# Optimization experiments

Hardware: AMD Instinct MI355X
Metric: run time of the kernel (lower is better)

The kernel has to match this reference:

```python
import jax, jax.numpy as jnp
import numpy as np
from jax import lax

# --- Clifford algebra Cl(3,0): sig_g = [1,1,1], n_blades = 8 ---
SIG = np.array([1.0, 1.0, 1.0], dtype=np.float32)
N_GEN = len(SIG)
N_BLADES = 1 << N_GEN

def _build_cayley(g):
    # Structure constants C[a,b,c]: e_a * e_b = C[a,b,a^b] * e_{a^b}
    n = len(g); nb = 1 << n
    C = np.zeros((nb, nb, nb), dtype=np.float32)
    for a in range(nb):
        for b in range(nb):
            s = 1.0
            x = a >> 1
            while x:
                if bin(x & b).count('1') % 2:
                    s = -s
                x >>= 1
            common = a & b
            for k in range(n):
                if (common >> k) & 1:
                    s *= g[k]
            C[a, b, a ^ b] = s
    return C

CAYLEY = _build_cayley(SIG)
# blade signs: scalar coefficient of e_i * e_i (metric square of each blade)
BLADE_SIGNS = np.array([CAYLEY[i, i, 0] for i in range(N_BLADES)], dtype=np.float32)

DT = 0.1      # EPEngine dt
N_FREE = 5    # EPEngine n_free

def _energy(h, input_mv, W_rec, C, signs):
    # h: [B,L,H,I]
    rho = jnp.clip(h, 0.0, 1.0)
    E_self = 0.5 * jnp.sum(h * h, axis=(1, 2, 3))                       # [B]
    E_in = jnp.einsum('blhi,blhi,i->b', rho, input_mv, signs)           # [B]
    # causal recurrent term: geometric product of h_{l-1} with W_rec
    rec = jnp.einsum('blhi,ghj,ijk->blgk', rho[:, :-1], W_rec, C)       # [B,L-1,H,I]
    E_rec = jnp.einsum('blhk,blhk,k->b', rho[:, 1:], rec, signs)        # [B]
    return E_self - E_in - E_rec

def _free_phase(h0, input_mv, W_rec, C, signs):
    gfn = jax.grad(lambda h: jnp.sum(_energy(h, input_mv, W_rec, C, signs)))
    def step(h, _):
        return h - DT * gfn(h), None
    h, _ = lax.scan(step, h0, None, length=N_FREE)
    return h

def setup_inputs() -> dict:
    key = jax.random.key(0)
    ks = jax.random.split(key, 5)
    B, L, V, E, H = 4, 256, 32000, 256, 256
    x = jax.random.randint(ks[0], (B, L), 0, V)
    emb_table = jax.random.normal(ks[1], (V, E), jnp.float32)
    W_in = jax.random.normal(ks[2], (H, E, N_BLADES), jnp.float32) * 0.1
    W_rec = jax.random.normal(ks[3], (H, H, N_BLADES), jnp.float32) * 0.05
    W_out = jax.random.normal(ks[4], (V, H, N_BLADES), jnp.float32) * 0.1
    return {"x": x, "emb_table": emb_table, "W_in": W_in, "W_rec": W_rec, "W_out": W_out}

def reference(x, emb_table, W_in, W_rec, W_out):
    C = jnp.asarray(CAYLEY)
    signs = jnp.asarray(BLADE_SIGNS)
    emb = emb_table[x]                                  # [B,L,E]
    input_mv = jnp.einsum('bld,hdi->blhi', emb, W_in)   # [B,L,H,I]
    B, L = x.shape
    H = W_in.shape[0]
    h0 = jnp.zeros((B, L, H, N_BLADES), jnp.float32)
    h_free = _free_phase(h0, input_mv, W_rec, C, signs) # [B,L,H,I]
    # scalar part of geometric product of h_free with W_out (only blade 0 kept)
    logits = jnp.einsum('blhi,vhj,ij->blv', h_free, W_out, C[:, :, 0])
    return logits
```

## Files before the change

kernel.cpp:

```cpp
#include <hip/hip_runtime.h>
#include <cstddef>
#include <cstdint>

#define VOCAB  32000
#define EMB    256
#define NB     8
#define KDIM   2048
#define NROWS  1024
#define NCOL   4096
#define LLEN   256

typedef __attribute__((ext_vector_type(8))) short short8;
typedef __attribute__((ext_vector_type(4))) float f32x4;
typedef __attribute__((ext_vector_type(16))) float f32x16;
typedef __attribute__((ext_vector_type(4))) int i32x4;
typedef __attribute__((ext_vector_type(16))) int i32x16;

__device__ __forceinline__ float cl3_sign(int a, int b) {
  int x = a >> 1, p = 0;
  while (x) { p ^= __popc(x & b) & 1; x >>= 1; }
  return p ? -1.f : 1.f;
}

__device__ __forceinline__ float clipf(float v) { return fminf(fmaxf(v, 0.f), 1.f); }

__device__ __forceinline__ unsigned short f2bf(float f) {
  unsigned u = __float_as_uint(f);
  u += 0x7FFF + ((u >> 16) & 1);
  return (unsigned short)(u >> 16);
}
__device__ __forceinline__ float bf2f(unsigned short h) {
  return __uint_as_float(((unsigned)h) << 16);
}

__device__ __forceinline__ size_t tso128(int tr, int tk, int r, int kk) {
  return ((size_t)(tr * 64 + tk) << 12) + ((size_t)((kk >> 3) & 3) << 10) + (r << 3) + (kk & 7);
}

__device__ __forceinline__ void gload16(const void* g, void* l) {
  __builtin_amdgcn_global_load_lds((const __attribute__((address_space(1))) uint32_t*)g,
                                   (__attribute__((address_space(3))) uint32_t*)l, 16, 0, 0);
}

__device__ __forceinline__ float dig_inv(float mx) {
  return exp2f((float)(5 - ilogbf(fmaxf(mx, 1e-20f))));
}

__global__ void k_build_mrt_split(const float* __restrict__ Wrec,
                                  unsigned short* __restrict__ Mhi,
                                  unsigned short* __restrict__ Mlo) {
  int idx = blockIdx.x * blockDim.x + threadIdx.x;
  int k = idx & (KDIM - 1);
  int n = idx >> 11;
  int h = k >> 3, i = k & 7;
  float v;
  if (n < KDIM) {
    int g = n >> 3, kb = n & 7;
    int j = i ^ kb;
    v = Wrec[(size_t)g * KDIM + h * NB + j] * cl3_sign(i, j);
  } else {
    int c = n - KDIM;
    int p = c >> 3, q = c & 7;
    int j = q ^ i;
    v = cl3_sign(i, i) * cl3_sign(q, j) * Wrec[(size_t)h * KDIM + p * NB + j];
  }
  unsigned short hi = f2bf(v);
  unsigned short lo = f2bf(v - bf2f(hi));
  size_t off = tso128(n >> 7, k >> 5, n & 127, k & 31);
  Mhi[off] = hi; Mlo[off] = lo;
}

__global__ __launch_bounds__(256) void k_wout_max(const float* __restrict__ W, float* __restrict__ scl) {
  __shared__ float red[256];
  const int t = threadIdx.x;
  size_t stride = (size_t)gridDim.x * 256;
  float m = 0.f;
  for (size_t i = (size_t)blockIdx.x * 256 + t; i < (size_t)VOCAB * KDIM / 4; i += stride) {
    float4 v = ((const float4*)W)[i];
    m = fmaxf(m, fmaxf(fmaxf(fabsf(v.x), fabsf(v.y)), fmaxf(fabsf(v.z), fabsf(v.w))));
  }
  red[t] = m; __syncthreads();
  for (int s = 128; s; s >>= 1) { if (t < s) red[t] = fmaxf(red[t], red[t + s]); __syncthreads(); }
  if (t == 0) atomicMax((unsigned*)(scl + 1), __float_as_uint(red[0]));
}

__global__ __launch_bounds__(256) void k_dig_wout(const float* __restrict__ W,
                                                  const float* __restrict__ scl,
                                                  char* __restrict__ Wd1,
                                                  char* __restrict__ Wd2) {
  __shared__ char l1[16384], l2[16384];
  const int tn = blockIdx.x >> 5;
  const int kt = blockIdx.x & 31;
  const int t = threadIdx.x;
  const float inv = dig_inv(scl[1]);
#pragma unroll
  for (int p = 0; p < 8; ++p) {
    int ci = p * 256 + t;
    int row = ci >> 3, koff = (ci & 7) * 8;
    const float* src = W + (size_t)(tn * 256 + row) * KDIM + kt * 64 + koff;
    float e[8];
    *(float4*)&e[0] = *(const float4*)src;
    *(float4*)&e[4] = *(const float4*)(src + 4);
    char d1[8], d2[8];
#pragma unroll
    for (int j = 0; j < 8; ++j) {
      float tv = e[j] * inv;
      float f1 = rintf(tv);
      d1[j] = (char)(int)f1;
      d2[j] = (char)(int)rintf((tv - f1) * 128.f);
    }
    int lo = ((koff >> 4) << 12) + (row << 4) + (koff & 8);
    *(uint64_t*)&l1[lo] = *(uint64_t*)d1;
    *(uint64_t*)&l2[lo] = *(uint64_t*)d2;
  }
  __syncthreads();
  size_t ob = ((size_t)blockIdx.x << 14) + t * 64;
#pragma unroll
  for (int q = 0; q < 4; ++q) {
    *(i32x4*)&Wd1[ob + q * 16] = *(const i32x4*)&l1[t * 64 + q * 16];
    *(i32x4*)&Wd2[ob + q * 16] = *(const i32x4*)&l2[t * 64 + q * 16];
  }
}

__global__ __launch_bounds__(256) void k_input_mv(const int* __restrict__ x,
                                                  const float* __restrict__ emb,
                                                  const float* __restrict__ Win,
                                                  float* __restrict__ out) {
  __shared__ float se[4][EMB];
  int r0 = blockIdx.x * 4;
  int t = threadIdx.x;
  for (int rr = 0; rr < 4; ++rr) {
    int tok = x[r0 + rr];
    se[rr][t] = emb[(size_t)tok * EMB + t];
  }
  __syncthreads();
  float acc[4][8];
#pragma unroll
  for (int rr = 0; rr < 4; ++rr)
#pragma unroll
    for (int i = 0; i < 8; ++i) acc[rr][i] = 0.f;
  const float* wrow = Win + (size_t)t * KDIM;
  for (int d = 0; d < EMB; ++d) {
    float4 w0 = *(const float4*)(wrow + d * 8);
    float4 w1 = *(const float4*)(wrow + d * 8 + 4);
#pragma unroll
    for (int rr = 0; rr < 4; ++rr) {
      float e = se[rr][d];
      acc[rr][0] += e * w0.x; acc[rr][1] += e * w0.y;
      acc[rr][2] += e * w0.z; acc[rr][3] += e * w0.w;
      acc[rr][4] += e * w1.x; acc[rr][5] += e * w1.y;
      acc[rr][6] += e * w1.z; acc[rr][7] += e * w1.w;
    }
  }
  for (int rr = 0; rr < 4; ++rr) {
    float4* o = (float4*)(out + (size_t)(r0 + rr) * KDIM + t * 8);
    o[0] = make_float4(acc[rr][0], acc[rr][1], acc[rr][2], acc[rr][3]);
    o[1] = make_float4(acc[rr][4], acc[rr][5], acc[rr][6], acc[rr][7]);
  }
}

__global__ __launch_bounds__(256, 2) void k_gemm_pre(const unsigned short* __restrict__ Ahi,
                                                     const unsigned short* __restrict__ Alo,
                                                     const unsigned short* __restrict__ Bhi,
                                                     const unsigned short* __restrict__ Blo,
                                                     float* __restrict__ RF0,
                                                     float* __restrict__ RF1) {
  __shared__ __align__(16) unsigned short lds[2][4][4096];
  const int b = blockIdx.x;
  const int lin = (b & 7) * 64 + (b >> 3);
  const int half = lin >> 8;
  const int inner = lin & 255;
  const int tn = inner >> 3, tm = inner & 7;
  const int ktbase = half << 5;
  float* __restrict__ C = half ? RF1 : RF0;
  const int t = threadIdx.x;
  const int l = t & 63, w = t >> 6;
  const int wr = w >> 1, wc = w & 1;

  const unsigned short* aH = Ahi + ((size_t)tm * 64 << 12);
  const unsigned short* aL = Alo + ((size_t)tm * 64 << 12);
  const unsigned short* bH = Bhi + ((size_t)tn * 64 << 12);
  const unsigned short* bL = Blo + ((size_t)tn * 64 << 12);

  const int ldso0 = w * 1024;
  const int ldso1 = ldso0 + 512;
  const int srco0 = ldso0 + (l << 3);
  const int srco1 = ldso1 + (l << 3);

  const int rA0 = wr * 64 + (l & 31);
  const int rB0 = wc * 64 + (l & 31);
  const int ch0 = l >> 5;

  f32x16 acc[2][2];
#pragma unroll
  for (int i = 0; i < 2; ++i)
#pragma unroll
    for (int j = 0; j < 2; ++j) acc[i][j] = (f32x16)0.f;

  auto STAGE = [&](int bf, int kt) {
    size_t kb = (size_t)kt << 12;
    gload16(aH + kb + srco0, &lds[bf][0][ldso0]);
    gload16(aH + kb + srco1, &lds[bf][0][ldso1]);
    gload16(aL + kb + srco0, &lds[bf][1][ldso0]);
    gload16(aL + kb + srco1, &lds[bf][1][ldso1]);
    gload16(bH + kb + srco0, &lds[bf][2][ldso0]);
    gload16(bH + kb + srco1, &lds[bf][2][ldso1]);
    gload16(bL + kb + srco0, &lds[bf][3][ldso0]);
    gload16(bL + kb + srco1, &lds[bf][3][ldso1]);
  };

  STAGE(0, ktbase);
  __syncthreads();
  int cur = 0;
  for (int it = 0; it < 32; ++it) {
    if (it < 31) STAGE(cur ^ 1, ktbase + it + 1);
#pragma unroll
    for (int s = 0; s < 2; ++s) {
      const int cb = (s * 2 + ch0) << 10;
      short8 ah[2], al[2], bh[2], bl[2];
#pragma unroll
      for (int mi = 0; mi < 2; ++mi) {
        ah[mi] = *(const short8*)&lds[cur][0][cb + ((rA0 + mi * 32) << 3)];
        al[mi] = *(const short8*)&lds[cur][1][cb + ((rA0 + mi * 32) << 3)];
      }
#pragma unroll
      for (int nj = 0; nj < 2; ++nj) {
        bh[nj] = *(const short8*)&lds[cur][2][cb + ((rB0 + nj * 32) << 3)];
        bl[nj] = *(const short8*)&lds[cur][3][cb + ((rB0 + nj * 32) << 3)];
      }
#pragma unroll
      for (int mi = 0; mi < 2; ++mi)
#pragma unroll
        for (int nj = 0; nj < 2; ++nj) {
          acc[mi][nj] = __builtin_amdgcn_mfma_f32_32x32x16_bf16(ah[mi], bh[nj], acc[mi][nj], 0, 0, 0);
          acc[mi][nj] = __builtin_amdgcn_mfma_f32_32x32x16_bf16(ah[mi], bl[nj], acc[mi][nj], 0, 0, 0);
          acc[mi][nj] = __builtin_amdgcn_mfma_f32_32x32x16_bf16(al[mi], bh[nj], acc[mi][nj], 0, 0, 0);
        }
    }
    __syncthreads();
    cur ^= 1;
  }

  const int rg0 = tm * 128 + wr * 64 + ((l >> 5) << 2);
  const int cg0 = tn * 128 + wc * 64 + (l & 31);
#pragma unroll
  for (int mi = 0; mi < 2; ++mi)
#pragma unroll
    for (int nj = 0; nj < 2; ++nj) {
      f32x16 v = acc[mi][nj];
#pragma unroll
      for (int g = 0; g < 16; ++g) {
        int rr = (g & 3) + ((g >> 2) << 3);
        C[(size_t)(rg0 + mi * 32 + rr) * NCOL + cg0 + nj * 32] = v[g];
      }
    }
}

__global__ __launch_bounds__(512, 1) void k_gemm_i8(const char* __restrict__ Ad1,
                                                    const char* __restrict__ Ad2,
                                                    const char* __restrict__ Bd1,
                                                    const char* __restrict__ Bd2,
                                                    const float* __restrict__ scl,
                                                    const float* __restrict__ sA,
                                                    float* __restrict__ C) {
  __shared__ __align__(16) char lds[3 * 49152];
  const int b = blockIdx.x;
  const int lin = (b & 7) * 125 + (b >> 3);
  const int tm = lin & 7, tn = lin >> 3;
  const int t = threadIdx.x;
  const int l = t & 63, w = t >> 6;
  const int wr = w >> 2, wc = w & 3;

  const char* a1g = Ad1 + ((size_t)tm * 32 << 13) + (t << 4);
  const char* a2g = Ad2 + ((size_t)tm * 32 << 13) + (t << 4);
  const char* b1g = Bd1 + ((size_t)tn * 32 << 14) + (t << 4);
  const char* b2g = Bd2 + ((size_t)tn * 32 << 14) + (t << 4);
  const int wub = w << 10;

  const int la = (l & 31) << 4;
  const int rowa0 = (wr * 64 + 0) << 4, rowa1 = (wr * 64 + 32) << 4;
  const int rowb0 = (wc * 64 + 0) << 4, rowb1 = (wc * 64 + 32) << 4;
  const int kqh = (l >> 5) << 1;

  i32x16 acc1[2][2], acc2[2][2];
#pragma unroll
  for (int i = 0; i < 2; ++i)
#pragma unroll
    for (int j = 0; j < 2; ++j) { acc1[i][j] = (i32x16)0; acc2[i][j] = (i32x16)0; }

  auto STAGE_H = [&](int bf, int kt, int h) {
    char* lb = &lds[bf * 49152];
    size_t ka = (size_t)kt << 13, kb = (size_t)kt << 14;
    if (h == 0) {
      gload16(a1g + ka, lb + wub);
      gload16(a2g + ka, lb + 8192 + wub);
      gload16(b1g + kb, lb + 16384 + wub);
    } else {
      gload16(b1g + kb + 8192, lb + 24576 + wub);
      gload16(b2g + kb, lb + 32768 + wub);
      gload16(b2g + kb + 8192, lb + 40960 + wub);
    }
  };

  STAGE_H(0, 0, 0); STAGE_H(0, 0, 1);
  STAGE_H(1, 1, 0); STAGE_H(1, 1, 1);

  int cur = 0;
  for (int kt = 0; kt < 32; ++kt) {
    int pf = cur + 2; if (pf >= 3) pf -= 3;
    if (kt < 31) { asm volatile("s_waitcnt vmcnt(6)" ::: "memory"); }
    else         { asm volatile("s_waitcnt vmcnt(0)" ::: "memory"); }
    __builtin_amdgcn_s_barrier();
    const char* lb = &lds[cur * 49152];
#pragma unroll
    for (int s = 0; s < 2; ++s) {
      const int kqa = ((s << 1) + (l >> 5)) << 11;
      const int kqb = ((s << 1) + (l >> 5)) << 12;
      i32x4 a1[2], a2[2], b1[2], b2[2];
      a1[0] = *(const i32x4*)(lb + kqa + rowa0 + la);
      a1[1] = *(const i32x4*)(lb + kqa + rowa1 + la);
      a2[0] = *(const i32x4*)(lb + 8192 + kqa + rowa0 + la);
      a2[1] = *(const i32x4*)(lb + 8192 + kqa + rowa1 + la);
      b1[0] = *(const i32x4*)(lb + 16384 + kqb + rowb0 + la);
      b1[1] = *(const i32x4*)(lb + 16384 + kqb + rowb1 + la);
      b2[0] = *(const i32x4*)(lb + 32768 + kqb + rowb0 + la);
      b2[1] = *(const i32x4*)(lb + 32768 + kqb + rowb1 + la);
      if (kt + 2 < 32) STAGE_H(pf, kt + 2, s);
      __builtin_amdgcn_s_setprio(1);
#pragma unroll
      for (int mi = 0; mi < 2; ++mi)
#pragma unroll
        for (int nj = 0; nj < 2; ++nj) {
          acc1[mi][nj] = __builtin_amdgcn_mfma_i32_32x32x32_i8(a1[mi], b1[nj], acc1[mi][nj], 0, 0, 0);
          acc2[mi][nj] = __builtin_amdgcn_mfma_i32_32x32x32_i8(a1[mi], b2[nj], acc2[mi][nj], 0, 0, 0);
          acc2[mi][nj] = __builtin_amdgcn_mfma_i32_32x32x32_i8(a2[mi], b1[nj], acc2[mi][nj], 0, 0, 0);
        }
      __builtin_amdgcn_s_setprio(0);
    }
    cur = (cur == 2) ? 0 : cur + 1;
  }

  const float sB = exp2f((float)(ilogbf(scl[1]) + 2));
  const int rbase = tm * 128 + wr * 64 + ((l >> 5) << 2);
  const int cbase = tn * 256 + wc * 64 + (l & 31);
#pragma unroll
  for (int mi = 0; mi < 2; ++mi)
#pragma unroll
    for (int nj = 0; nj < 2; ++nj) {
#pragma unroll
      for (int g = 0; g < 16; ++g) {
        int rr = (g & 3) + ((g >> 2) << 3);
        int row = rbase + mi * 32 + rr;
        float c1 = sA[row] * sB * (1.f / 16384.f);
        C[(size_t)row * VOCAB + cbase + nj * 32] =
            fmaf((float)acc2[mi][nj][g], c1 * (1.f / 128.f), (float)acc1[mi][nj][g] * c1);
      }
    }
}

template <int LAST>
__global__ __launch_bounds__(256) void k_update(float* __restrict__ Hb, const float* __restrict__ Imv,
                                                const float* __restrict__ RF0, const float* __restrict__ RF1,
                                                unsigned short* __restrict__ Hhi,
                                                unsigned short* __restrict__ Hlo,
                                                float* __restrict__ sA,
                                                char* __restrict__ Ad1,
                                                char* __restrict__ Ad2,
                                                int big) {
  __shared__ float red[256];
  int tix = threadIdx.x;
  int idx = blockIdx.x * 256 + tix;
  int r = idx >> 8;
  int c = (idx & 255) << 3;
  int m = r & (LLEN - 1);
  const size_t base = (size_t)r * KDIM + c;
  float h[8], f[8];
  *(float4*)&h[0] = *(const float4*)(Hb + base);
  *(float4*)&h[4] = *(const float4*)(Hb + base + 4);
  float4 i0 = *(const float4*)(Imv + base);
  float4 i1 = *(const float4*)(Imv + base + 4);
  f[0] = i0.x; f[1] = i0.y; f[2] = i0.z; f[3] = i0.w;
  f[4] = i1.x; f[5] = i1.y; f[6] = i1.z; f[7] = i1.w;
#pragma unroll
  for (int j = 0; j < 8; ++j) f[j] *= ((0xE8 >> j) & 1) ? -1.f : 1.f;
  if (m >= 1) {
    const float* rp0 = RF0 + (size_t)(r - 1) * NCOL + c;
    const float* rp1 = RF1 + (size_t)(r - 1) * NCOL + c;
#pragma unroll
    for (int j = 0; j < 8; ++j)
      f[j] += (rp0[j] + rp1[j]) * (((0xE8 >> j) & 1) ? -1.f : 1.f);
  }
  if (m < LLEN - 1) {
    const float* rn0 = RF0 + (size_t)(r + 1) * NCOL + KDIM + c;
    const float* rn1 = RF1 + (size_t)(r + 1) * NCOL + KDIM + c;
#pragma unroll
    for (int j = 0; j < 8; ++j) f[j] += rn0[j] + rn1[j];
  }
  float hn[8], av[8];
#pragma unroll
  for (int j = 0; j < 8; ++j) {
    float hv = h[j];
    float dr = (hv > 0.f && hv < 1.f) ? 1.f : ((hv == 0.f || hv == 1.f) ? 0.5f : 0.f);
    hn[j] = hv - 0.1f * (hv - dr * f[j]);
  }
  *(float4*)(Hb + base) = make_float4(hn[0], hn[1], hn[2], hn[3]);
  *(float4*)(Hb + base + 4) = make_float4(hn[4], hn[5], hn[6], hn[7]);
  if (!LAST) {
    short8 h8, l8;
#pragma unroll
    for (int j = 0; j < 8; ++j) {
      float a = clipf(hn[j]);
      unsigned short hi = f2bf(a);
      h8[j] = (short)hi;
      l8[j] = (short)f2bf(a - bf2f(hi));
    }
    size_t off = tso128(r >> 7, c >> 5, r & 127, c & 31);
    *(short8*)&Hhi[off] = h8;
    *(short8*)&Hlo[off] = l8;
  } else {
    if (!big) return;
#pragma unroll
    for (int j = 0; j < 8; ++j) av[j] = hn[j] * (((0xE8 >> j) & 1) ? -1.f : 1.f);
    float lm = 0.f;
#pragma unroll
    for (int j = 0; j < 8; ++j) lm = fmaxf(lm, fabsf(av[j]));
    red[tix] = lm; __syncthreads();
    for (int s = 128; s; s >>= 1) { if (tix < s) red[tix] = fmaxf(red[tix], red[tix + s]); __syncthreads(); }
    float mx = fmaxf(red[0], 1e-20f);
    float inv = dig_inv(mx);
    if (tix == 0) sA[r] = exp2f((float)(ilogbf(mx) + 2));
    char d1[8], d2[8];
#pragma unroll
    for (int j = 0; j < 8; ++j) {
      float tv = av[j] * inv;
      float f1 = rintf(tv);
      d1[j] = (char)(int)f1;
      d2[j] = (char)(int)rintf((tv - f1) * 128.f);
    }
    size_t addr = (((size_t)(r >> 7) * 32 + (tix >> 3)) << 13) + ((size_t)((tix >> 1) & 3) << 11)
                + ((r & 127) << 4) + ((tix & 1) << 3);
    *(uint64_t*)&Ad1[addr] = *(uint64_t*)d1;
    *(uint64_t*)&Ad2[addr] = *(uint64_t*)d2;
  }
}

template <int AMODE>
__global__ __launch_bounds__(256) void k_gemm_split(const float* __restrict__ A,
                                                    const float* __restrict__ B,
                                                    float* __restrict__ C, int ldc) {
  __shared__ unsigned short Ah[128 * 32], Al[128 * 32];
  __shared__ unsigned short Bh[128 * 32], Bl[128 * 32];
  const int t = threadIdx.x;
  const int row0 = blockIdx.y * 128, col0 = blockIdx.x * 128;
  const int l = t & 63, w = t >> 6;
  const int wr = w >> 1, wc = w & 1;
  const int sr = t >> 3;
  const int cc = (t & 7) << 2;
  const int chunkb = cc >> 3;
  const int halfo = (cc >> 2) & 1;
  f32x4 acc[4][4];
#pragma unroll
  for (int i = 0; i < 4; ++i)
#pragma unroll
    for (int j = 0; j < 4; ++j) acc[i][j] = (f32x4)0.f;
  const float sA0 = 1.f;
  const float sA1 = (cc & 4) ? -1.f : 1.f;
  const float sA2 = sA1;
  const float sA3 = -1.f;
  for (int k0 = 0; k0 < KDIM; k0 += 32) {
    float4 va[4], vb[4];
#pragma unroll
    for (int i = 0; i < 4; ++i) {
      va[i] = *(const float4*)(A + (size_t)(row0 + sr + i * 32) * KDIM + k0 + cc);
      vb[i] = *(const float4*)(B + (size_t)(col0 + sr + i * 32) * KDIM + k0 + cc);
    }
    __syncthreads();
#pragma unroll
    for (int i = 0; i < 4; ++i) {
      int row = sr + i * 32;
      int idx = row * 32 + ((chunkb ^ (row & 3)) << 3) + (halfo << 2);
      float4 a = va[i];
      if (AMODE == 0) {
        a.x = clipf(a.x); a.y = clipf(a.y); a.z = clipf(a.z); a.w = clipf(a.w);
      } else {
        a.x *= sA0; a.y *= sA1; a.z *= sA2; a.w *= sA3;
      }
      ushort4 h4, l4;
      h4.x = f2bf(a.x); l4.x = f2bf(a.x - bf2f(h4.x));
      h4.y = f2bf(a.y); l4.y = f2bf(a.y - bf2f(h4.y));
      h4.z = f2bf(a.z); l4.z = f2bf(a.z - bf2f(h4.z));
      h4.w = f2bf(a.w); l4.w = f2bf(a.w - bf2f(h4.w));
      *(ushort4*)&Ah[idx] = h4;
      *(ushort4*)&Al[idx] = l4;
      float4 bb = vb[i];
      h4.x = f2bf(bb.x); l4.x = f2bf(bb.x - bf2f(h4.x));
      h4.y = f2bf(bb.y); l4.y = f2bf(bb.y - bf2f(h4.y));
      h4.z = f2bf(bb.z); l4.z = f2bf(bb.z - bf2f(h4.z));
      h4.w = f2bf(bb.w); l4.w = f2bf(bb.w - bf2f(h4.w));
      *(ushort4*)&Bh[idx] = h4;
      *(ushort4*)&Bl[idx] = l4;
    }
    __syncthreads();
    short8 ah[4], al[4], bh[4], bl[4];
#pragma unroll
    for (int mi = 0; mi < 4; ++mi) {
      int ar = wr * 64 + mi * 16 + (l & 15);
      int kc = (l >> 4) ^ (ar & 3);
      ah[mi] = *(short8*)&Ah[ar * 32 + kc * 8];
      al[mi] = *(short8*)&Al[ar * 32 + kc * 8];
      int br = wc * 64 + mi * 16 + (l & 15);
      int kb = (l >> 4) ^ (br & 3);
      bh[mi] = *(short8*)&Bh[br * 32 + kb * 8];
      bl[mi] = *(short8*)&Bl[br * 32 + kb * 8];
    }
#pragma unroll
    for (int mi = 0; mi < 4; ++mi)
#pragma unroll
      for (int ni = 0; ni < 4; ++ni) {
        acc[mi][ni] = __builtin_amdgcn_mfma_f32_16x16x32_bf16(ah[mi], bh[ni], acc[mi][ni], 0, 0, 0);
        acc[mi][ni] = __builtin_amdgcn_mfma_f32_16x16x32_bf16(ah[mi], bl[ni], acc[mi][ni], 0, 0, 0);
        acc[mi][ni] = __builtin_amdgcn_mfma_f32_16x16x32_bf16(al[mi], bh[ni], acc[mi][ni], 0, 0, 0);
      }
  }
#pragma unroll
  for (int mi = 0; mi < 4; ++mi)
#pragma unroll
    for (int ni = 0; ni < 4; ++ni) {
      int rg = row0 + wr * 64 + mi * 16 + (l >> 4) * 4;
      int cg = col0 + wc * 64 + ni * 16 + (l & 15);
#pragma unroll
      for (int j = 0; j < 4; ++j)
        C[(size_t)(rg + j) * ldc + cg] = acc[mi][ni][j];
    }
}

extern "C" void kernel_launch(void* const* d_in, const int* in_sizes, int n_in,
                              void* d_out, int out_size, void* d_ws, size_t ws_size,
                              hipStream_t stream) {
  const int*   x    = (const int*)d_in[0];
  const float* emb  = (const float*)d_in[1];
  const float* Win  = (const float*)d_in[2];
  const float* Wrec = (const float*)d_in[3];
  const float* Wout = (const float*)d_in[4];
  float* logits = (float*)d_out;

  char* base = (char*)d_ws;
  const size_t MB = 1ull << 20;
  float* Hbuf = (float*)(base + 0);
  float* Imv  = (float*)(base + 8 * MB);
  float* RF0  = (float*)(base + 16 * MB);
  float* RF1  = (float*)(base + 32 * MB);
  unsigned short* Hhi = (unsigned short*)(base + 48 * MB);
  unsigned short* Hlo = (unsigned short*)(base + 52 * MB);
  unsigned short* Mhi = (unsigned short*)(base + 56 * MB);
  unsigned short* Mlo = (unsigned short*)(base + 72 * MB);
  float* scl = (float*)(base + 88 * MB);
  float* sA  = (float*)(base + 88 * MB + 4096);
  char* Wd1  = base + 88 * MB + 8192;
  char* Wd2  = Wd1 + (size_t)VOCAB * KDIM;
  char* Ad1  = (char*)Mhi;
  char* Ad2  = (char*)Mlo;

  const size_t need = (size_t)(Wd2 - base) + (size_t)VOCAB * KDIM;
  const bool big = ws_size >= need;

  hipMemsetAsync(Hbuf, 0, 8 * MB, stream);
  hipMemsetAsync(Hhi, 0, 8 * MB, stream);
  if (big) hipMemsetAsync(scl, 0, 16, stream);
  k_build_mrt_split<<<32768, 256, 0, stream>>>(Wrec, Mhi, Mlo);
  k_input_mv<<<256, 256, 0, stream>>>(x, emb, Win, Imv);
  if (big) {
    k_wout_max<<<2048, 256, 0, stream>>>(Wout, scl);
    k_dig_wout<<<4000, 256, 0, stream>>>(Wout, scl, Wd1, Wd2);
  }

  for (int it = 0; it < 5; ++it) {
    k_gemm_pre<<<512, 256, 0, stream>>>(Hhi, Hlo, Mhi, Mlo, RF0, RF1);
    if (it < 4) k_update<0><<<1024, 256, 0, stream>>>(Hbuf, Imv, RF0, RF1, Hhi, Hlo, sA, Ad1, Ad2, big);
    else        k_update<1><<<1024, 256, 0, stream>>>(Hbuf, Imv, RF0, RF1, Hhi, Hlo, sA, Ad1, Ad2, big);
  }

  if (big) {
    k_gemm_i8<<<1000, 512, 0, stream>>>(Ad1, Ad2, Wd1, Wd2, scl, sA, logits);
  } else {
    k_gemm_split<1><<<dim3(VOCAB / 128, NROWS / 128), 256, 0, stream>>>(Hbuf, Wout, logits, VOCAB);
  }
}
```

Baseline: 750.5 us.

## Use per-row Wout scales, fuse max into digitize, retile GEMMs with triple buffering

Drops the separate global max-reduction pass over Wout. k_dig_wout now computes a per-row scale in the same pass that digitizes each row to int8 pairs, which removes one full read of the 262MB weight. It also changes the operand layouts to 16-wide k chunks. The recurrent bf16 GEMM moves to three-stage LDS buffering with vmcnt waits, one barrier per step and setprio. The final int8 GEMM goes from 128x256 tiles with 512 threads to 128x128 tiles with 256 threads and two blocks per CU. Per-row scaling should also tighten quantization, but the smaller tiles raise reuse pressure and double the number of blocks.

```diff
diff --git a/kernel.cpp b/kernel.cpp
--- a/kernel.cpp
+++ b/kernel.cpp
@@ -33,10 +33,6 @@
   return __uint_as_float(((unsigned)h) << 16);
 }
 
-__device__ __forceinline__ size_t tso128(int tr, int tk, int r, int kk) {
-  return ((size_t)(tr * 64 + tk) << 12) + ((size_t)((kk >> 3) & 3) << 10) + (r << 3) + (kk & 7);
-}
-
 __device__ __forceinline__ void gload16(const void* g, void* l) {
   __builtin_amdgcn_global_load_lds((const __attribute__((address_space(1))) uint32_t*)g,
                                    (__attribute__((address_space(3))) uint32_t*)l, 16, 0, 0);
@@ -44,6 +40,10 @@
 
 __device__ __forceinline__ float dig_inv(float mx) {
   return exp2f((float)(5 - ilogbf(fmaxf(mx, 1e-20f))));
+}
+
+__device__ __forceinline__ size_t bfoff(int rt, int k, int r) {
+  return ((size_t)(rt * 128 + (k >> 4)) << 11) + (size_t)(((k >> 3) & 1) << 10) + ((r & 127) << 3) + (k & 7);
 }
 
 __global__ void k_build_mrt_split(const float* __restrict__ Wrec,
@@ -66,41 +66,36 @@
   }
   unsigned short hi = f2bf(v);
   unsigned short lo = f2bf(v - bf2f(hi));
-  size_t off = tso128(n >> 7, k >> 5, n & 127, k & 31);
+  size_t off = bfoff(n >> 7, k, n);
   Mhi[off] = hi; Mlo[off] = lo;
 }
 
-__global__ __launch_bounds__(256) void k_wout_max(const float* __restrict__ W, float* __restrict__ scl) {
-  __shared__ float red[256];
-  const int t = threadIdx.x;
-  size_t stride = (size_t)gridDim.x * 256;
-  float m = 0.f;
-  for (size_t i = (size_t)blockIdx.x * 256 + t; i < (size_t)VOCAB * KDIM / 4; i += stride) {
-    float4 v = ((const float4*)W)[i];
-    m = fmaxf(m, fmaxf(fmaxf(fabsf(v.x), fabsf(v.y)), fmaxf(fabsf(v.z), fabsf(v.w))));
-  }
-  red[t] = m; __syncthreads();
-  for (int s = 128; s; s >>= 1) { if (t < s) red[t] = fmaxf(red[t], red[t + s]); __syncthreads(); }
-  if (t == 0) atomicMax((unsigned*)(scl + 1), __float_as_uint(red[0]));
-}
-
 __global__ __launch_bounds__(256) void k_dig_wout(const float* __restrict__ W,
-                                                  const float* __restrict__ scl,
+                                                  float* __restrict__ sB,
                                                   char* __restrict__ Wd1,
                                                   char* __restrict__ Wd2) {
-  __shared__ char l1[16384], l2[16384];
-  const int tn = blockIdx.x >> 5;
-  const int kt = blockIdx.x & 31;
   const int t = threadIdx.x;
-  const float inv = dig_inv(scl[1]);
-#pragma unroll
-  for (int p = 0; p < 8; ++p) {
-    int ci = p * 256 + t;
-    int row = ci >> 3, koff = (ci & 7) * 8;
-    const float* src = W + (size_t)(tn * 256 + row) * KDIM + kt * 64 + koff;
+  const int row = blockIdx.x * 32 + (t >> 3);
+  const int g = t & 7;
+  const float* src = W + (size_t)row * KDIM + g * 256;
+  float m = 0.f;
+#pragma unroll 8
+  for (int q = 0; q < 64; ++q) {
+    float4 v = *(const float4*)(src + q * 4);
+    m = fmaxf(m, fmaxf(fmaxf(fabsf(v.x), fabsf(v.y)), fmaxf(fabsf(v.z), fabsf(v.w))));
+  }
+  m = fmaxf(m, __shfl_xor(m, 1));
+  m = fmaxf(m, __shfl_xor(m, 2));
+  m = fmaxf(m, __shfl_xor(m, 4));
+  m = fmaxf(m, 1e-20f);
+  if (g == 0) sB[row] = exp2f((float)(ilogbf(m) + 2));
+  const float inv = dig_inv(m);
+  const int tn = row >> 7, rowin = row & 127;
+  for (int q = 0; q < 32; ++q) {
+    int c = g * 256 + q * 8;
     float e[8];
-    *(float4*)&e[0] = *(const float4*)src;
-    *(float4*)&e[4] = *(const float4*)(src + 4);
+    *(float4*)&e[0] = *(const float4*)(src + q * 8);
+    *(float4*)&e[4] = *(const float4*)(src + q * 8 + 4);
     char d1[8], d2[8];
 #pragma unroll
     for (int j = 0; j < 8; ++j) {
@@ -109,16 +104,10 @@
       d1[j] = (char)(int)f1;
       d2[j] = (char)(int)rintf((tv - f1) * 128.f);
     }
-    int lo = ((koff >> 4) << 12) + (row << 4) + (koff & 8);
-    *(uint64_t*)&l1[lo] = *(uint64_t*)d1;
-    *(uint64_t*)&l2[lo] = *(uint64_t*)d2;
-  }
-  __syncthreads();
-  size_t ob = ((size_t)blockIdx.x << 14) + t * 64;
-#pragma unroll
-  for (int q = 0; q < 4; ++q) {
-    *(i32x4*)&Wd1[ob + q * 16] = *(const i32x4*)&l1[t * 64 + q * 16];
-    *(i32x4*)&Wd2[ob + q * 16] = *(const i32x4*)&l2[t * 64 + q * 16];
+    size_t addr = ((size_t)(tn * 64 + (c >> 5)) << 12) + (size_t)(((c >> 4) & 1) << 11)
+                + (rowin << 4) + (c & 15);
+    *(uint64_t*)&Wd1[addr] = *(uint64_t*)d1;
+    *(uint64_t*)&Wd2[addr] = *(uint64_t*)d2;
   }
 }
 
@@ -165,31 +154,23 @@
                                                      const unsigned short* __restrict__ Blo,
                                                      float* __restrict__ RF0,
                                                      float* __restrict__ RF1) {
-  __shared__ __align__(16) unsigned short lds[2][4][4096];
+  __shared__ __align__(16) char lds[3 * 16384];
   const int b = blockIdx.x;
   const int lin = (b & 7) * 64 + (b >> 3);
   const int half = lin >> 8;
-  const int inner = lin & 255;
-  const int tn = inner >> 3, tm = inner & 7;
-  const int ktbase = half << 5;
+  const int rest = lin & 255;
+  const int tm = rest & 7, tn = rest >> 3;
+  const int ktbase = half * 64;
   float* __restrict__ C = half ? RF1 : RF0;
   const int t = threadIdx.x;
   const int l = t & 63, w = t >> 6;
   const int wr = w >> 1, wc = w & 1;
 
-  const unsigned short* aH = Ahi + ((size_t)tm * 64 << 12);
-  const unsigned short* aL = Alo + ((size_t)tm * 64 << 12);
-  const unsigned short* bH = Bhi + ((size_t)tn * 64 << 12);
-  const unsigned short* bL = Blo + ((size_t)tn * 64 << 12);
-
-  const int ldso0 = w * 1024;
-  const int ldso1 = ldso0 + 512;
-  const int srco0 = ldso0 + (l << 3);
-  const int srco1 = ldso1 + (l << 3);
-
-  const int rA0 = wr * 64 + (l & 31);
-  const int rB0 = wc * 64 + (l & 31);
-  const int ch0 = l >> 5;
+  const char* aHg = (const char*)Ahi + (((size_t)tm * 128 + ktbase) << 12) + (t << 4);
+  const char* aLg = (const char*)Alo + (((size_t)tm * 128 + ktbase) << 12) + (t << 4);
+  const char* bHg = (const char*)Bhi + (((size_t)tn * 128 + ktbase) << 12) + (t << 4);
+  const char* bLg = (const char*)Blo + (((size_t)tn * 128 + ktbase) << 12) + (t << 4);
+  const int wo = w << 10;
 
   f32x16 acc[2][2];
 #pragma unroll
@@ -198,47 +179,51 @@
     for (int j = 0; j < 2; ++j) acc[i][j] = (f32x16)0.f;
 
   auto STAGE = [&](int bf, int kt) {
+    char* lb = &lds[bf * 16384];
     size_t kb = (size_t)kt << 12;
-    gload16(aH + kb + srco0, &lds[bf][0][ldso0]);
-    gload16(aH + kb + srco1, &lds[bf][0][ldso1]);
-    gload16(aL + kb + srco0, &lds[bf][1][ldso0]);
-    gload16(aL + kb + srco1, &lds[bf][1][ldso1]);
-    gload16(bH + kb + srco0, &lds[bf][2][ldso0]);
-    gload16(bH + kb + srco1, &lds[bf][2][ldso1]);
-    gload16(bL + kb + srco0, &lds[bf][3][ldso0]);
-    gload16(bL + kb + srco1, &lds[bf][3][ldso1]);
+    gload16(aHg + kb, lb + wo);
+    gload16(aLg + kb, lb + 4096 + wo);
+    gload16(bHg + kb, lb + 8192 + wo);
+    gload16(bLg + kb, lb + 12288 + wo);
   };
 
-  STAGE(0, ktbase);
-  __syncthreads();
+  STAGE(0, 0); STAGE(1, 1);
+
+  const int ra = wr * 64 + (l & 31);
+  const int rb = wc * 64 + (l & 31);
+  const int cho = (l >> 5) << 11;
   int cur = 0;
-  for (int it = 0; it < 32; ++it) {
-    if (it < 31) STAGE(cur ^ 1, ktbase + it + 1);
-#pragma unroll
-    for (int s = 0; s < 2; ++s) {
-      const int cb = (s * 2 + ch0) << 10;
-      short8 ah[2], al[2], bh[2], bl[2];
-#pragma unroll
-      for (int mi = 0; mi < 2; ++mi) {
-        ah[mi] = *(const short8*)&lds[cur][0][cb + ((rA0 + mi * 32) << 3)];
-        al[mi] = *(const short8*)&lds[cur][1][cb + ((rA0 + mi * 32) << 3)];
+  for (int kt = 0; kt < 64; ++kt) {
+    int pf = cur + 2; if (pf >= 3) pf -= 3;
+    if (kt < 63) { asm volatile("s_waitcnt vmcnt(4)" ::: "memory"); }
+    else         { asm volatile("s_waitcnt vmcnt(0)" ::: "memory"); }
+    __builtin_amdgcn_s_barrier();
+    const char* lb = &lds[cur * 16384];
+    short8 ah[2], al[2], bh[2], bl[2];
+#pragma unroll
+    for (int mi = 0; mi < 2; ++mi) {
+      int off = cho + ((ra + mi * 32) << 4);
+      ah[mi] = *(const short8*)(lb + off);
+      al[mi] = *(const short8*)(lb + 4096 + off);
+    }
+#pragma unroll
+    for (int nj = 0; nj < 2; ++nj) {
+      int off = cho + ((rb + nj * 32) << 4);
+      bh[nj] = *(const short8*)(lb + 8192 + off);
+      bl[nj] = *(const short8*)(lb + 12288 + off);
+    }
+    if (kt + 2 < 64) STAGE(pf, kt + 2);
+    __builtin_amdgcn_s_setprio(1);
+#pragma unroll
+    for (int mi = 0; mi < 2; ++mi)
+#pragma unroll
+      for (int nj = 0; nj < 2; ++nj) {
+        acc[mi][nj] = __builtin_amdgcn_mfma_f32_32x32x16_bf16(ah[mi], bh[nj], acc[mi][nj], 0, 0, 0);
+        acc[mi][nj] = __builtin_amdgcn_mfma_f32_32x32x16_bf16(ah[mi], bl[nj], acc[mi][nj], 0, 0, 0);
+        acc[mi][nj] = __builtin_amdgcn_mfma_f32_32x32x16_bf16(al[mi], bh[nj], acc[mi][nj], 0, 0, 0);
       }
-#pragma unroll
-      for (int nj = 0; nj < 2; ++nj) {
-        bh[nj] = *(const short8*)&lds[cur][2][cb + ((rB0 + nj * 32) << 3)];
-        bl[nj] = *(const short8*)&lds[cur][3][cb + ((rB0 + nj * 32) << 3)];
-      }
-#pragma unroll
-      for (int mi = 0; mi < 2; ++mi)
-#pragma unroll
-        for (int nj = 0; nj < 2; ++nj) {
-          acc[mi][nj] = __builtin_amdgcn_mfma_f32_32x32x16_bf16(ah[mi], bh[nj], acc[mi][nj], 0, 0, 0);
-          acc[mi][nj] = __builtin_amdgcn_mfma_f32_32x32x16_bf16(ah[mi], bl[nj], acc[mi][nj], 0, 0, 0);
-          acc[mi][nj] = __builtin_amdgcn_mfma_f32_32x32x16_bf16(al[mi], bh[nj], acc[mi][nj], 0, 0, 0);
-        }
-    }
-    __syncthreads();
-    cur ^= 1;
+    __builtin_amdgcn_s_setprio(0);
+    cur = (cur == 2) ? 0 : cur + 1;
   }
 
   const int rg0 = tm * 128 + wr * 64 + ((l >> 5) << 2);
@@ -256,31 +241,26 @@
     }
 }
 
-__global__ __launch_bounds__(512, 1) void k_gemm_i8(const char* __restrict__ Ad1,
+__global__ __launch_bounds__(256, 2) void k_gemm_i8(const char* __restrict__ Ad1,
                                                     const char* __restrict__ Ad2,
                                                     const char* __restrict__ Bd1,
                                                     const char* __restrict__ Bd2,
-                                                    const float* __restrict__ scl,
                                                     const float* __restrict__ sA,
+                                                    const float* __restrict__ sB,
                                                     float* __restrict__ C) {
-  __shared__ __align__(16) char lds[3 * 49152];
+  __shared__ __align__(16) char lds[3 * 16384];
   const int b = blockIdx.x;
-  const int lin = (b & 7) * 125 + (b >> 3);
+  const int lin = (b & 7) * 250 + (b >> 3);
   const int tm = lin & 7, tn = lin >> 3;
   const int t = threadIdx.x;
   const int l = t & 63, w = t >> 6;
-  const int wr = w >> 2, wc = w & 3;
-
-  const char* a1g = Ad1 + ((size_t)tm * 32 << 13) + (t << 4);
-  const char* a2g = Ad2 + ((size_t)tm * 32 << 13) + (t << 4);
-  const char* b1g = Bd1 + ((size_t)tn * 32 << 14) + (t << 4);
-  const char* b2g = Bd2 + ((size_t)tn * 32 << 14) + (t << 4);
-  const int wub = w << 10;
-
-  const int la = (l & 31) << 4;
-  const int rowa0 = (wr * 64 + 0) << 4, rowa1 = (wr * 64 + 32) << 4;
-  const int rowb0 = (wc * 64 + 0) << 4, rowb1 = (wc * 64 + 32) << 4;
-  const int kqh = (l >> 5) << 1;
+  const int wr = w >> 1, wc = w & 1;
+
+  const char* a1g = Ad1 + (((size_t)tm * 64) << 12) + (t << 4);
+  const char* a2g = Ad2 + (((size_t)tm * 64) << 12) + (t << 4);
+  const char* b1g = Bd1 + (((size_t)tn * 64) << 12) + (t << 4);
+  const char* b2g = Bd2 + (((size_t)tn * 64) << 12) + (t << 4);
+  const int wo = w << 10;
 
   i32x16 acc1[2][2], acc2[2][2];
 #pragma unroll
@@ -288,71 +268,67 @@
 #pragma unroll
     for (int j = 0; j < 2; ++j) { acc1[i][j] = (i32x16)0; acc2[i][j] = (i32x16)0; }
 
-  auto STAGE_H = [&](int bf, int kt, int h) {
-    char* lb = &lds[bf * 49152];
-    size_t ka = (size_t)kt << 13, kb = (size_t)kt << 14;
-    if (h == 0) {
-      gload16(a1g + ka, lb + wub);
-      gload16(a2g + ka, lb + 8192 + wub);
-      gload16(b1g + kb, lb + 16384 + wub);
-    } else {
-      gload16(b1g + kb + 8192, lb + 24576 + wub);
-      gload16(b2g + kb, lb + 32768 + wub);
-      gload16(b2g + kb + 8192, lb + 40960 + wub);
-    }
+  auto STAGE = [&](int bf, int kt) {
+    char* lb = &lds[bf * 16384];
+    size_t kb = (size_t)kt << 12;
+    gload16(a1g + kb, lb + wo);
+    gload16(a2g + kb, lb + 4096 + wo);
+    gload16(b1g + kb, lb + 8192 + wo);
+    gload16(b2g + kb, lb + 12288 + wo);
   };
 
-  STAGE_H(0, 0, 0); STAGE_H(0, 0, 1);
-  STAGE_H(1, 1, 0); STAGE_H(1, 1, 1);
-
+  STAGE(0, 0); STAGE(1, 1);
+
+  const int ra = wr * 64 + (l & 31);
+  const int rb = wc * 64 + (l & 31);
+  const int kqo = (l >> 5) << 11;
   int cur = 0;
-  for (int kt = 0; kt < 32; ++kt) {
+  for (int kt = 0; kt < 64; ++kt) {
     int pf = cur + 2; if (pf >= 3) pf -= 3;
-    if (kt < 31) { asm volatile("s_waitcnt vmcnt(6)" ::: "memory"); }
+    if (kt < 63) { asm volatile("s_waitcnt vmcnt(4)" ::: "memory"); }
     else         { asm volatile("s_waitcnt vmcnt(0)" ::: "memory"); }
     __builtin_amdgcn_s_barrier();
-    const char* lb = &lds[cur * 49152];
-#pragma unroll
-    for (int s = 0; s < 2; ++s) {
-      const int kqa = ((s << 1) + (l >> 5)) << 11;
-      const int kqb = ((s << 1) + (l >> 5)) << 12;
-      i32x4 a1[2], a2[2], b1[2], b2[2];
-      a1[0] = *(const i32x4*)(lb + kqa + rowa0 + la);
-      a1[1] = *(const i32x4*)(lb + kqa + rowa1 + la);
-      a2[0] = *(const i32x4*)(lb + 8192 + kqa + rowa0 + la);
-      a2[1] = *(const i32x4*)(lb + 8192 + kqa + rowa1 + la);
-      b1[0] = *(const i32x4*)(lb + 16384 + kqb + rowb0 + la);
-      b1[1] = *(const i32x4*)(lb + 16384 + kqb + rowb1 + la);
-      b2[0] = *(const i32x4*)(lb + 32768 + kqb + rowb0 + la);
-      b2[1] = *(const i32x4*)(lb + 32768 + kqb + rowb1 + la);
-      if (kt + 2 < 32) STAGE_H(pf, kt + 2, s);
-      __builtin_amdgcn_s_setprio(1);
-#pragma unroll
-      for (int mi = 0; mi < 2; ++mi)
-#pragma unroll
-        for (int nj = 0; nj < 2; ++nj) {
-          acc1[mi][nj] = __builtin_amdgcn_mfma_i32_32x32x32_i8(a1[mi], b1[nj], acc1[mi][nj], 0, 0, 0);
-          acc2[mi][nj] = __builtin_amdgcn_mfma_i32_32x32x32_i8(a1[mi], b2[nj], acc2[mi][nj], 0, 0, 0);
-          acc2[mi][nj] = __builtin_amdgcn_mfma_i32_32x32x32_i8(a2[mi], b1[nj], acc2[mi][nj], 0, 0, 0);
-        }
-      __builtin_amdgcn_s_setprio(0);
-    }
+    const char* lb = &lds[cur * 16384];
+    i32x4 a1[2], a2[2], b1[2], b2[2];
+#pragma unroll
+    for (int mi = 0; mi < 2; ++mi) {
+      int off = kqo + ((ra + mi * 32) << 4);
+      a1[mi] = *(const i32x4*)(lb + off);
+      a2[mi] = *(const i32x4*)(lb + 4096 + off);
+    }
+#pragma unroll
+    for (int nj = 0; nj < 2; ++nj) {
+      int off = kqo + ((rb + nj * 32) << 4);
+      b1[nj] = *(const i32x4*)(lb + 8192 + off);
+      b2[nj] = *(const i32x4*)(lb + 12288 + off);
+    }
+    if (kt + 2 < 64) STAGE(pf, kt + 2);
+    __builtin_amdgcn_s_setprio(1);
+#pragma unroll
+    for (int mi = 0; mi < 2; ++mi)
+#pragma unroll
+      for (int nj = 0; nj < 2; ++nj) {
+        acc1[mi][nj] = __builtin_amdgcn_mfma_i32_32x32x32_i8(a1[mi], b1[nj], acc1[mi][nj], 0, 0, 0);
+        acc2[mi][nj] = __builtin_amdgcn_mfma_i32_32x32x32_i8(a1[mi], b2[nj], acc2[mi][nj], 0, 0, 0);
+        acc2[mi][nj] = __builtin_amdgcn_mfma_i32_32x32x32_i8(a2[mi], b1[nj], acc2[mi][nj], 0, 0, 0);
+      }
+    __builtin_amdgcn_s_setprio(0);
     cur = (cur == 2) ? 0 : cur + 1;
   }
 
-  const float sB = exp2f((float)(ilogbf(scl[1]) + 2));
   const int rbase = tm * 128 + wr * 64 + ((l >> 5) << 2);
-  const int cbase = tn * 256 + wc * 64 + (l & 31);
+  const int cb = tn * 128 + wc * 64 + (l & 31);
 #pragma unroll
   for (int mi = 0; mi < 2; ++mi)
 #pragma unroll
     for (int nj = 0; nj < 2; ++nj) {
+      float sBv = sB[cb + nj * 32] * (1.f / 16384.f);
 #pragma unroll
       for (int g = 0; g < 16; ++g) {
         int rr = (g & 3) + ((g >> 2) << 3);
         int row = rbase + mi * 32 + rr;
-        float c1 = sA[row] * sB * (1.f / 16384.f);
-        C[(size_t)row * VOCAB + cbase + nj * 32] =
+        float c1 = sA[row] * sBv;
+        C[(size_t)row * VOCAB + cb + nj * 32] =
             fmaf((float)acc2[mi][nj][g], c1 * (1.f / 128.f), (float)acc1[mi][nj][g] * c1);
       }
     }
@@ -414,7 +390,7 @@
       h8[j] = (short)hi;
       l8[j] = (short)f2bf(a - bf2f(hi));
     }
-    size_t off = tso128(r >> 7, c >> 5, r & 127, c & 31);
+    size_t off = bfoff(r >> 7, c, r);
     *(short8*)&Hhi[off] = h8;
     *(short8*)&Hlo[off] = l8;
   } else {
@@ -437,8 +413,8 @@
       d1[j] = (char)(int)f1;
       d2[j] = (char)(int)rintf((tv - f1) * 128.f);
     }
-    size_t addr = (((size_t)(r >> 7) * 32 + (tix >> 3)) << 13) + ((size_t)((tix >> 1) & 3) << 11)
-                + ((r & 127) << 4) + ((tix & 1) << 3);
+    size_t addr = ((size_t)((r >> 7) * 64 + (c >> 5)) << 12) + (size_t)(((c >> 4) & 1) << 11)
+                + ((r & 127) << 4) + (c & 15);
     *(uint64_t*)&Ad1[addr] = *(uint64_t*)d1;
     *(uint64_t*)&Ad2[addr] = *(uint64_t*)d2;
   }
@@ -554,9 +530,9 @@
   unsigned short* Hlo = (unsigned short*)(base + 52 * MB);
   unsigned short* Mhi = (unsigned short*)(base + 56 * MB);
   unsigned short* Mlo = (unsigned short*)(base + 72 * MB);
-  float* scl = (float*)(base + 88 * MB);
-  float* sA  = (float*)(base + 88 * MB + 4096);
-  char* Wd1  = base + 88 * MB + 8192;
+  float* sA  = (float*)(base + 88 * MB);
+  float* sB  = (float*)(base + 88 * MB + 4096);
+  char* Wd1  = base + 88 * MB + 160 * 1024;
   char* Wd2  = Wd1 + (size_t)VOCAB * KDIM;
   char* Ad1  = (char*)Mhi;
   char* Ad2  = (char*)Mlo;
@@ -566,12 +542,10 @@
 
   hipMemsetAsync(Hbuf, 0, 8 * MB, stream);
   hipMemsetAsync(Hhi, 0, 8 * MB, stream);
-  if (big) hipMemsetAsync(scl, 0, 16, stream);
   k_build_mrt_split<<<32768, 256, 0, stream>>>(Wrec, Mhi, Mlo);
   k_input_mv<<<256, 256, 0, stream>>>(x, emb, Win, Imv);
   if (big) {
-    k_wout_max<<<2048, 256, 0, stream>>>(Wout, scl);
-    k_dig_wout<<<4000, 256, 0, stream>>>(Wout, scl, Wd1, Wd2);
+    k_dig_wout<<<1000, 256, 0, stream>>>(Wout, sB, Wd1, Wd2);
   }
 
   for (int it = 0; it < 5; ++it) {
@@ -581,7 +555,7 @@
   }
 
   if (big) {
-    k_gemm_i8<<<1000, 512, 0, stream>>>(Ad1, Ad2, Wd1, Wd2, scl, sA, logits);
+    k_gemm_i8<<<2000, 256, 0, stream>>>(Ad1, Ad2, Wd1, Wd2, sA, sB, logits);
   } else {
     k_gemm_split<1><<<dim3(VOCAB / 128, NROWS / 128), 256, 0, stream>>>(Hbuf, Wout, logits, VOCAB);
   }
```

After: 846.5 us. +12.8%, slower.
